# Kernel tuning notes

Measured on AMD Instinct MI355X. Metric: run time of the kernel, lower is better.

## Reference

```python
import jax, jax.numpy as jnp
import numpy as np

T = 0.07        # temperature (hardcoded in CCM)
BN_EPS = 1e-5   # torch BatchNorm1d default eps (eval mode, running stats)


def _l2norm(x):
    # torch F.normalize(dim=1): x / max(||x||, 1e-12)
    n = jnp.linalg.norm(x, axis=1, keepdims=True)
    return x / jnp.maximum(n, 1e-12)


def _attn(q, k):
    # cosine similarity scaled by 1/t and 1/sqrt(num_keys)
    scale = jnp.asarray(k.shape[0], q.dtype) ** 0.5
    return (_l2norm(q) @ _l2norm(k).T) / T / scale


def setup_inputs() -> dict:
    key = jax.random.key(0)
    ks = jax.random.split(key, 24)
    D, N, BS, C, H = 2048, 1024, 64, 65, 128
    f32 = jnp.float32
    def g(k, shape, scale=1.0):
        return jax.random.normal(k, shape, f32) * scale
    return {
        "all_f": g(ks[0], (BS, D)),
        "embedding": _l2norm(g(ks[1], (N, D))),  # memory queue (normalized at init)
        "all_y": jax.random.randint(ks[2], (BS,), 0, C),
        "head_w1": g(ks[3], (D, H), 1.0 / np.sqrt(D)),
        "head_b1": jnp.zeros((H,), f32),
        "head_g": jax.random.uniform(ks[4], (H,), f32) + 0.5,
        "head_beta": g(ks[5], (H,), 0.1),
        "head_rm": g(ks[6], (H,), 0.1),
        "head_rv": jax.random.uniform(ks[7], (H,), f32) + 0.5,
        "head_w2": g(ks[8], (H, H), 1.0 / np.sqrt(H)),
        "head_b2": jnp.zeros((H,), f32),
        "mix_w1": g(ks[9], (2 * H, H), 1.0 / np.sqrt(2 * H)),
        "mix_b1": jnp.zeros((H,), f32),
        "mix_g": jax.random.uniform(ks[10], (H,), f32) + 0.5,
        "mix_beta": g(ks[11], (H,), 0.1),
        "mix_rm": g(ks[12], (H,), 0.1),
        "mix_rv": jax.random.uniform(ks[13], (H,), f32) + 0.5,
        "mix_w2": g(ks[14], (H, D), 1.0 / np.sqrt(H)),
        "mix_b2": jnp.zeros((D,), f32),
        "clf_w": g(ks[15], (D, C), 1.0 / np.sqrt(D)),
        "clf_b": jnp.zeros((C,), f32),
    }


def reference(all_f, embedding, all_y,
              head_w1, head_b1, head_g, head_beta, head_rm, head_rv, head_w2, head_b2,
              mix_w1, mix_b1, mix_g, mix_beta, mix_rm, mix_rv, mix_w2, mix_b2,
              clf_w, clf_b):
    # CCM.causal(all_f, embedding, all_y): returns [bs, num_classes]
    H = head_b2.shape[0]
    # z|x attention over the memory queue
    z_x = jax.nn.softmax(_attn(all_f, embedding), axis=-1)          # [bs, N]

    def head(x):
        h = x @ head_w1 + head_b1
        h = (h - head_rm) * jax.lax.rsqrt(head_rv + BN_EPS) * head_g + head_beta
        return jax.nn.relu(h) @ head_w2 + head_b2                   # [., 128]

    hf = head(all_f)        # [bs, 128]
    hz = head(embedding)    # [N, 128]
    # mixer layer 1 on concat([hf, hz]) decomposed into two matmuls + broadcast add
    h1 = hf @ mix_w1[:H] + mix_b1                                   # [bs, 128]
    h1 = h1[:, None, :] + (hz @ mix_w1[H:])[None, :, :]             # [bs, N, 128]
    h1 = (h1 - mix_rm) * jax.lax.rsqrt(mix_rv + BN_EPS) * mix_g + mix_beta
    h1 = jax.nn.relu(h1)
    mixed = h1 @ mix_w2 + mix_b2                                    # [bs, N, D]
    y_zx = jax.nn.softmax(mixed @ clf_w + clf_b, axis=-1)           # [bs, N, C] = p(y|z,x)
    # p(x): self-attention row-sums, softmax over the batch (all_y given -> this branch)
    p_x = jax.nn.softmax(_attn(all_f, all_f).sum(axis=1), axis=0)   # [bs]
    sum_x = jnp.einsum('b,bnc->nc', p_x, y_zx)                      # [N, C]
    return z_x @ sum_x                                              # [bs, C]
```

## Files before the change

### kernel.cpp

```cpp
#include <hip/hip_runtime.h>
#include <hip/hip_bf16.h>
#include <math.h>

#define D   2048
#define NQ  1024
#define BSZ 64
#define NC  65
#define HD  128

#define OFF_SCALEH 0
#define OFF_CH     128
#define OFF_BZC    256
#define OFF_BAC    384
#define OFF_BVEC   512
#define OFF_PXP    640
#define OFF_WC     896
#define OFF_SP     145280
#define OFF_SUMX   669568
#define OFF_FNB    751488
#define OFF_AFB    817024
#define OFF_EMBB   882560
#define OFF_W1T    1931136
#define OFF_WZT    2062208
#define OFF_WAT    2070400
#define OFF_MW2B   2078592
#define OFF_CWT    2226048
#define OFF_H1P    2307968

typedef __attribute__((ext_vector_type(8))) short    bf16x8;
typedef __attribute__((ext_vector_type(4))) float    f32x4;
typedef __attribute__((ext_vector_type(8))) unsigned short u16x8;
typedef __attribute__((ext_vector_type(2))) unsigned short u16x2;

__device__ inline unsigned short f2b(float v) {
    __hip_bfloat16 h = __float2bfloat16(v);
    return __builtin_bit_cast(unsigned short, h);
}
__device__ inline float bf2f(unsigned short u) {
    return __builtin_bit_cast(float, ((unsigned)u) << 16);
}

__global__ void __launch_bounds__(256) k_prep(const float* __restrict__ all_f,
                                              const float* __restrict__ emb,
                                              const float* __restrict__ head_w1,
                                              const float* __restrict__ head_b1,
                                              const float* __restrict__ head_g,
                                              const float* __restrict__ head_beta,
                                              const float* __restrict__ head_rm,
                                              const float* __restrict__ head_rv,
                                              const float* __restrict__ head_w2,
                                              const float* __restrict__ head_b2,
                                              const float* __restrict__ mix_w1,
                                              const float* __restrict__ mix_b1,
                                              const float* __restrict__ mix_g,
                                              const float* __restrict__ mix_beta,
                                              const float* __restrict__ mix_rm,
                                              const float* __restrict__ mix_rv,
                                              const float* __restrict__ mix_w2,
                                              const float* __restrict__ mix_b2,
                                              const float* __restrict__ clf_w,
                                              float* __restrict__ ws) {
    __shared__ float sbuf[128*66];
    int bid = blockIdx.x, t = threadIdx.x;
    if (bid == 0) {
        int h = t & 127, jq = t >> 7;
        float sb = 0.f, sa = 0.f;
        #pragma unroll 8
        for (int j = jq*64; j < jq*64 + 64; ++j) {
            float b2v = head_b2[j];
            sb = fmaf(b2v, mix_w1[(HD + j)*HD + h], sb);
            sa = fmaf(b2v, mix_w1[j*HD + h], sa);
        }
        sbuf[jq*256 + h]       = sb;
        sbuf[jq*256 + 128 + h] = sa;
        __syncthreads();
        if (jq == 0) {
            float s = head_g[h] * rsqrtf(head_rv[h] + 1e-5f);
            ws[OFF_SCALEH + h] = s;
            ws[OFF_CH + h] = (head_b1[h] - head_rm[h]) * s + head_beta[h];
            float ms = mix_g[h] * rsqrtf(mix_rv[h] + 1e-5f);
            float msh = mix_beta[h] - mix_rm[h] * ms;
            float sbT = sbuf[h] + sbuf[256 + h];
            float saT = sbuf[128 + h] + sbuf[256 + 128 + h];
            ws[OFF_BZC + h] = sbT * ms;
            ws[OFF_BAC + h] = fmaf(saT + mix_b1[h], ms, msh);
        }
    } else if (bid < 129) {
        int j = bid - 1;
        int h = t & 127, which = t >> 7;
        const float* M1 = mix_w1 + (which ? 0 : HD*HD);
        float ms = mix_g[h] * rsqrtf(mix_rv[h] + 1e-5f);
        float acc = 0.f;
        #pragma unroll 8
        for (int k = 0; k < HD; ++k)
            acc = fmaf(head_w2[j*HD + k], M1[k*HD + h], acc);
        unsigned short* dst = (unsigned short*)(ws + (which ? OFF_WAT : OFF_WZT));
        dst[h*HD + j] = f2b(acc * ms);
    } else if (bid < 165) {
        int r0 = (bid - 129) * 4;
        unsigned short* dst = (unsigned short*)(ws + OFF_MW2B);
        int i0 = t * 8;
        for (int rr = 0; rr < 4; ++rr) {
            int r = r0 + rr;
            u16x8 o;
            if (r < HD || r == HD) {
                const float* src = (r < HD) ? (mix_w2 + (size_t)r * D) : mix_b2;
                float4 f1 = *(const float4*)(src + i0);
                float4 f2 = *(const float4*)(src + i0 + 4);
                o[0]=f2b(f1.x); o[1]=f2b(f1.y); o[2]=f2b(f1.z); o[3]=f2b(f1.w);
                o[4]=f2b(f2.x); o[5]=f2b(f2.y); o[6]=f2b(f2.z); o[7]=f2b(f2.w);
            } else {
                o[0]=0;o[1]=0;o[2]=0;o[3]=0;o[4]=0;o[5]=0;o[6]=0;o[7]=0;
            }
            *(u16x8*)(dst + (size_t)r*D + i0) = o;
        }
    } else if (bid < 181) {
        int k0 = (bid - 165) * 128;
        float (*tile)[66] = (float(*)[66])sbuf;
        for (int i = t; i < 128*65; i += 256) {
            int r = i / 65;
            tile[r][i - 65*r] = clf_w[(size_t)k0*65 + i];
        }
        __syncthreads();
        unsigned short* cwt = (unsigned short*)(ws + OFF_CWT);
        for (int idx = t; idx < 80*16; idx += 256) {
            int c = idx >> 4, kq = idx & 15;
            u16x8 v;
            #pragma unroll
            for (int j = 0; j < 8; ++j)
                v[j] = (c < NC) ? f2b(tile[kq*8 + j][c]) : (unsigned short)0;
            *(u16x8*)(cwt + (size_t)c*D + k0 + kq*8) = v;
        }
    } else if (bid < 245) {
        int b = bid - 181;
        const float* src = all_f + (size_t)b * D;
        int i0 = t * 8;
        float4 f1 = *(const float4*)(src + i0);
        float4 f2 = *(const float4*)(src + i0 + 4);
        float s = f1.x*f1.x + f1.y*f1.y + f1.z*f1.z + f1.w*f1.w
                + f2.x*f2.x + f2.y*f2.y + f2.z*f2.z + f2.w*f2.w;
        s += __shfl_xor(s, 1);  s += __shfl_xor(s, 2);  s += __shfl_xor(s, 4);
        s += __shfl_xor(s, 8);  s += __shfl_xor(s, 16); s += __shfl_xor(s, 32);
        if ((t & 63) == 0) sbuf[t >> 6] = s;
        __syncthreads();
        float tot = sbuf[0] + sbuf[1] + sbuf[2] + sbuf[3];
        float rn = 1.f / fmaxf(sqrtf(tot), 1e-12f);
        unsigned short* fnb = (unsigned short*)(ws + OFF_FNB) + (size_t)b * D;
        unsigned short* afb = (unsigned short*)(ws + OFF_AFB) + (size_t)b * D;
        u16x8 on, oa;
        on[0]=f2b(f1.x*rn); on[1]=f2b(f1.y*rn); on[2]=f2b(f1.z*rn); on[3]=f2b(f1.w*rn);
        on[4]=f2b(f2.x*rn); on[5]=f2b(f2.y*rn); on[6]=f2b(f2.z*rn); on[7]=f2b(f2.w*rn);
        oa[0]=f2b(f1.x); oa[1]=f2b(f1.y); oa[2]=f2b(f1.z); oa[3]=f2b(f1.w);
        oa[4]=f2b(f2.x); oa[5]=f2b(f2.y); oa[6]=f2b(f2.z); oa[7]=f2b(f2.w);
        *(u16x8*)(fnb + i0) = on;
        *(u16x8*)(afb + i0) = oa;
    } else if (bid < 757) {
        int n0 = (bid - 245) * 2;
        unsigned short* dst = (unsigned short*)(ws + OFF_EMBB);
        int i0 = t * 8;
        for (int r = 0; r < 2; ++r) {
            const float* src = emb + (size_t)(n0 + r) * D;
            float4 f1 = *(const float4*)(src + i0);
            float4 f2 = *(const float4*)(src + i0 + 4);
            u16x8 o;
            o[0]=f2b(f1.x); o[1]=f2b(f1.y); o[2]=f2b(f1.z); o[3]=f2b(f1.w);
            o[4]=f2b(f2.x); o[5]=f2b(f2.y); o[6]=f2b(f2.z); o[7]=f2b(f2.w);
            *(u16x8*)(dst + (size_t)(n0 + r)*D + i0) = o;
        }
    } else {
        int rb = bid - 757;
        float (*tile)[33] = (float(*)[33])sbuf;
        int k0 = (rb >> 2) * 128, h0 = (rb & 3) * 32;
        int hh = t & 31, kk = t >> 5;
        for (int r = 0; r < 16; ++r)
            tile[kk + r*8][hh] = head_w1[(size_t)(k0 + kk + r*8)*HD + h0 + hh];
        __syncthreads();
        unsigned short* dst = (unsigned short*)(ws + OFF_W1T);
        int kcol = (t & 63) * 2, hrow = t >> 6;
        for (int r = 0; r < 8; ++r) {
            int h = hrow + r*4;
            u16x2 v;
            v[0] = f2b(tile[kcol][h]);
            v[1] = f2b(tile[kcol + 1][h]);
            *(u16x2*)(dst + (size_t)(h0 + h)*D + k0 + kcol) = v;
        }
    }
}

__global__ void __launch_bounds__(512) k_main(const float* __restrict__ clf_b,
                                              float* __restrict__ ws) {
    __shared__ float part[2][32][128];
    __shared__ float wcp[8][16][16];
    int bid = blockIdx.x, t = threadIdx.x;
    int lane = t & 63, wv = t >> 6;
    int row16 = lane & 15, kgrp = lane >> 4;
    if (bid < 128) {
        const unsigned short* fnb  = (const unsigned short*)(ws + OFF_FNB);
        const unsigned short* embb = (const unsigned short*)(ws + OFF_EMBB);
        int nt = bid & 15, ks = bid >> 4;
        int b0 = (wv & 3) * 16;
        int n0 = nt*64 + (wv >> 2) * 32;
        const unsigned short* Ap = fnb  + (size_t)(b0 + row16)*D + ks*256 + kgrp*8;
        const unsigned short* B0 = embb + (size_t)(n0 + row16)*D + ks*256 + kgrp*8;
        const unsigned short* B1 = B0 + 16*D;
        f32x4 a0 = {0,0,0,0}, a1 = {0,0,0,0};
        #pragma unroll
        for (int s = 0; s < 8; ++s) {
            bf16x8 a = *(const bf16x8*)(Ap + s*32);
            a0 = __builtin_amdgcn_mfma_f32_16x16x32_bf16(a, *(const bf16x8*)(B0 + s*32), a0, 0, 0, 0);
            a1 = __builtin_amdgcn_mfma_f32_16x16x32_bf16(a, *(const bf16x8*)(B1 + s*32), a1, 0, 0, 0);
        }
        float* Sp = ws + OFF_SP + (size_t)ks * BSZ * NQ;
        #pragma unroll
        for (int r = 0; r < 4; ++r) {
            float* rowp = Sp + (size_t)(b0 + kgrp*4 + r)*NQ + n0;
            rowp[row16]      = a0[r];
            rowp[16 + row16] = a1[r];
        }
    } else if (bid < 196) {
        int role = bid - 128;
        int tile = role >> 1, kh = role & 1;
        bool isF = tile >= 32;
        const unsigned short* Arow = isF
            ? (const unsigned short*)(ws + OFF_AFB) + (size_t)(tile - 32) * 32 * D
            : (const unsigned short*)(ws + OFF_EMBB) + (size_t)tile * 32 * D;
        const unsigned short* w1t = (const unsigned short*)(ws + OFF_W1T);
        int hgrp = wv & 3, kq = wv >> 2;
        int koff = kh*1024 + kq*512;
        const unsigned short* Ap = Arow + (size_t)row16*D + koff + kgrp*8;
        const unsigned short* B0 = w1t + (size_t)(hgrp*32 + row16)*D + koff + kgrp*8;
        const unsigned short* B1 = B0 + 16*D;
        f32x4 h00 = {0,0,0,0}, h01 = {0,0,0,0}, h10 = {0,0,0,0}, h11 = {0,0,0,0};
        #pragma unroll 4
        for (int s = 0; s < 16; ++s) {
            bf16x8 a0 = *(const bf16x8*)(Ap + s*32);
            bf16x8 a1 = *(const bf16x8*)(Ap + 16*D + s*32);
            bf16x8 b0 = *(const bf16x8*)(B0 + s*32);
            bf16x8 b1 = *(const bf16x8*)(B1 + s*32);
            h00 = __builtin_amdgcn_mfma_f32_16x16x32_bf16(a0, b0, h00, 0, 0, 0);
            h01 = __builtin_amdgcn_mfma_f32_16x16x32_bf16(a0, b1, h01, 0, 0, 0);
            h10 = __builtin_amdgcn_mfma_f32_16x16x32_bf16(a1, b0, h10, 0, 0, 0);
            h11 = __builtin_amdgcn_mfma_f32_16x16x32_bf16(a1, b1, h11, 0, 0, 0);
        }
        int mb = kgrp*4, hc0 = hgrp*32 + row16, hc1 = hc0 + 16;
        #pragma unroll
        for (int r = 0; r < 4; ++r) {
            part[kq][mb + r][hc0]      = h00[r];
            part[kq][mb + r][hc1]      = h01[r];
            part[kq][16 + mb + r][hc0] = h10[r];
            part[kq][16 + mb + r][hc1] = h11[r];
        }
        __syncthreads();
        int row = t >> 4, c8 = (t & 15) * 8;
        float* dst = ws + OFF_H1P + (size_t)kh*1088*HD + (size_t)(tile*32 + row)*HD + c8;
        float4 o0, o1;
        o0.x = part[0][row][c8+0] + part[1][row][c8+0];
        o0.y = part[0][row][c8+1] + part[1][row][c8+1];
        o0.z = part[0][row][c8+2] + part[1][row][c8+2];
        o0.w = part[0][row][c8+3] + part[1][row][c8+3];
        o1.x = part[0][row][c8+4] + part[1][row][c8+4];
        o1.y = part[0][row][c8+5] + part[1][row][c8+5];
        o1.z = part[0][row][c8+6] + part[1][row][c8+6];
        o1.w = part[0][row][c8+7] + part[1][row][c8+7];
        *(float4*)dst = o0;
        *(float4*)(dst + 4) = o1;
    } else if (bid < 241) {
        int w = bid - 196;
        int mt = w / 5, ntile = w % 5;
        const unsigned short* mw2b = (const unsigned short*)(ws + OFF_MW2B);
        const unsigned short* cwt  = (const unsigned short*)(ws + OFF_CWT);
        const unsigned short* Ap = mw2b + (size_t)(mt*16 + row16)*D + wv*256 + kgrp*8;
        const unsigned short* Bp = cwt  + (size_t)(ntile*16 + row16)*D + wv*256 + kgrp*8;
        f32x4 acc = {0,0,0,0};
        #pragma unroll
        for (int s = 0; s < 8; ++s)
            acc = __builtin_amdgcn_mfma_f32_16x16x32_bf16(
                *(const bf16x8*)(Ap + s*32), *(const bf16x8*)(Bp + s*32), acc, 0, 0, 0);
        #pragma unroll
        for (int r = 0; r < 4; ++r)
            wcp[wv][kgrp*4 + r][row16] = acc[r];
        __syncthreads();
        if (t < 256) {
            int j = t >> 4, c16 = t & 15;
            float s = 0.f;
            #pragma unroll
            for (int q = 0; q < 8; ++q) s += wcp[q][j][c16];
            int jj = mt*16 + j, c = ntile*16 + c16;
            unsigned short* wct = (unsigned short*)(ws + OFF_WC);
            if (jj < HD)       wct[(size_t)c*HD + jj] = f2b(s);
            else if (jj == HD) ws[OFF_BVEC + c] = (c < NC) ? s + clf_b[c] : -1e30f;
        }
    } else {
        int pb = bid - 241;
        const unsigned short* fnb = (const unsigned short*)(ws + OFF_FNB);
        int bq = wv & 3, kq = (wv >> 2) + pb*2;
        int b0 = bq*16;
        const unsigned short* Ap = fnb + (size_t)(b0 + row16)*D + kq*512 + kgrp*8;
        const unsigned short* Bp = fnb + (size_t)row16*D + kq*512 + kgrp*8;
        f32x4 acc[4];
        #pragma unroll
        for (int nt = 0; nt < 4; ++nt) acc[nt] = (f32x4){0.f,0.f,0.f,0.f};
        #pragma unroll 2
        for (int s = 0; s < 16; ++s) {
            bf16x8 a = *(const bf16x8*)(Ap + s*32);
            #pragma unroll
            for (int nt = 0; nt < 4; ++nt)
                acc[nt] = __builtin_amdgcn_mfma_f32_16x16x32_bf16(
                    a, *(const bf16x8*)(Bp + (size_t)nt*16*D + s*32), acc[nt], 0, 0, 0);
        }
        #pragma unroll
        for (int r = 0; r < 4; ++r) {
            float v = acc[0][r] + acc[1][r] + acc[2][r] + acc[3][r];
            v += __shfl_xor(v, 1); v += __shfl_xor(v, 2);
            v += __shfl_xor(v, 4); v += __shfl_xor(v, 8);
            if (row16 == 0)
                ws[OFF_PXP + kq*64 + b0 + kgrp*4 + r] = v;
        }
    }
}

__global__ void __launch_bounds__(512, 4) k_mixfin(const float* __restrict__ ws,
                                                   float* __restrict__ wsw) {
    __shared__ unsigned short wcs[80][136];
    __shared__ unsigned short ushA[96][136];
    __shared__ unsigned short a2s[64][136];
    __shared__ unsigned short b2s[32][136];
    __shared__ float redp[8][80];
    int bid = blockIdx.x, t = threadIdx.x;
    int lane = t & 63, wv = t >> 6;
    int row16 = lane & 15, kgrp = lane >> 4;

    const unsigned short* wct = (const unsigned short*)(ws + OFF_WC);
    for (int i = t; i < 80*16; i += 512) {
        int r = i >> 4, cc = (i & 15) * 8;
        *(u16x8*)&wcs[r][cc] = *(const u16x8*)(wct + (size_t)r*HD + cc);
    }

    int tb = bid >> 4;
    int frow = t >> 4, fc8 = (t & 15) * 8;
    #pragma unroll
    for (int g = 0; g < 3; ++g) {
        int u = frow + g*32;
        int h1row = (u < 32) ? (tb*32 + u) : (1024 + (u - 32));
        const float* h0p = ws + OFF_H1P + (size_t)h1row*HD + fc8;
        const float* h1p = h0p + (size_t)1088*HD;
        #pragma unroll
        for (int j = 0; j < 8; ++j) {
            int col = fc8 + j;
            float v = h0p[j] + h1p[j];
            ushA[u][col] = f2b(fmaxf(fmaf(v, ws[OFF_SCALEH + col], ws[OFF_CH + col]), 0.f));
        }
    }

    const float invTS = 1.0f / (0.07f * 8.0f);
    float sv = (ws[OFF_PXP + lane] + ws[OFF_PXP + 64 + lane]
              + ws[OFF_PXP + 128 + lane] + ws[OFF_PXP + 192 + lane]) * invTS;
    float m2 = sv;
    m2 = fmaxf(m2, __shfl_xor(m2, 1));  m2 = fmaxf(m2, __shfl_xor(m2, 2));
    m2 = fmaxf(m2, __shfl_xor(m2, 4));  m2 = fmaxf(m2, __shfl_xor(m2, 8));
    m2 = fmaxf(m2, __shfl_xor(m2, 16)); m2 = fmaxf(m2, __shfl_xor(m2, 32));
    float e2 = __expf(sv - m2);
    float ssum = e2;
    ssum += __shfl_xor(ssum, 1);  ssum += __shfl_xor(ssum, 2);  ssum += __shfl_xor(ssum, 4);
    ssum += __shfl_xor(ssum, 8);  ssum += __shfl_xor(ssum, 16); ssum += __shfl_xor(ssum, 32);
    float px = e2 / ssum;
    float bvl[5];
    #pragma unroll
    for (int ct = 0; ct < 5; ++ct) bvl[ct] = ws[OFF_BVEC + ct*16 + row16];
    __syncthreads();

    #pragma unroll
    for (int i = 0; i < 3; ++i) {
        int task = wv + i*8;
        int rt6 = task >> 2, cg = task & 3;
        bool isF = rt6 >= 2;
        const unsigned short* wt = (const unsigned short*)(ws + (isF ? OFF_WAT : OFF_WZT));
        const unsigned short* W0 = wt + (size_t)(cg*32 + row16)*HD + kgrp*8;
        const unsigned short* W1b = W0 + 16*HD;
        f32x4 o0 = {0,0,0,0}, o1 = {0,0,0,0};
        #pragma unroll
        for (int s = 0; s < 4; ++s) {
            bf16x8 a = *(const bf16x8*)(&ushA[rt6*16 + row16][s*32 + kgrp*8]);
            o0 = __builtin_amdgcn_mfma_f32_16x16x32_bf16(a, *(const bf16x8*)(W0 + s*32), o0, 0, 0, 0);
            o1 = __builtin_amdgcn_mfma_f32_16x16x32_bf16(a, *(const bf16x8*)(W1b + s*32), o1, 0, 0, 0);
        }
        int hcA = cg*32 + row16, hcB = hcA + 16;
        int boff = isF ? OFF_BAC : OFF_BZC;
        float bz0 = ws[boff + hcA], bz1 = ws[boff + hcB];
        #pragma unroll
        for (int r = 0; r < 4; ++r) {
            int orow = rt6*16 + kgrp*4 + r;
            if (orow < 32) {
                b2s[orow][hcA] = f2b(o0[r] + bz0);
                b2s[orow][hcB] = f2b(o1[r] + bz1);
            } else {
                a2s[orow - 32][hcA] = f2b(o0[r] + bz0);
                a2s[orow - 32][hcB] = f2b(o1[r] + bz1);
            }
        }
    }
    __syncthreads();

    int bt = wv & 3, ng = wv >> 2;
    u16x8 a2f[4];
    #pragma unroll
    for (int kt = 0; kt < 4; ++kt)
        a2f[kt] = *(const u16x8*)&a2s[bt*16 + row16][kt*32 + kgrp*8];
    int b2row = (bid & 15)*2 + ng;
    bf16x8 af[4];
    #pragma unroll
    for (int kt = 0; kt < 4; ++kt) {
        u16x8 bv = *(const u16x8*)&b2s[b2row][kt*32 + kgrp*8];
        bf16x8 v;
        #pragma unroll
        for (int j = 0; j < 8; ++j)
            v[j] = (short)f2b(fmaxf(bf2f(a2f[kt][j]) + bf2f(bv[j]), 0.f));
        af[kt] = v;
    }
    f32x4 acc[5];
    #pragma unroll
    for (int ct = 0; ct < 5; ++ct) acc[ct] = (f32x4){0.f,0.f,0.f,0.f};
    #pragma unroll
    for (int ct = 0; ct < 5; ++ct)
        #pragma unroll
        for (int kt = 0; kt < 4; ++kt)
            acc[ct] = __builtin_amdgcn_mfma_f32_16x16x32_bf16(
                af[kt], *(const bf16x8*)(&wcs[ct*16 + row16][kt*32 + kgrp*8]),
                acc[ct], 0, 0, 0);
    float outp[5] = {0.f, 0.f, 0.f, 0.f, 0.f};
    #pragma unroll
    for (int r = 0; r < 4; ++r) {
        float v0 = acc[0][r] + bvl[0];
        float v1 = acc[1][r] + bvl[1];
        float v2 = acc[2][r] + bvl[2];
        float v3 = acc[3][r] + bvl[3];
        float v4 = acc[4][r] + bvl[4];
        float m = fmaxf(fmaxf(fmaxf(v0, v1), fmaxf(v2, v3)), v4);
        m = fmaxf(m, __shfl_xor(m, 1)); m = fmaxf(m, __shfl_xor(m, 2));
        m = fmaxf(m, __shfl_xor(m, 4)); m = fmaxf(m, __shfl_xor(m, 8));
        float e0 = __expf(v0 - m), e1 = __expf(v1 - m), e2v = __expf(v2 - m);
        float e3 = __expf(v3 - m), e4 = __expf(v4 - m);
        float s = e0 + e1 + e2v + e3 + e4;
        s += __shfl_xor(s, 1); s += __shfl_xor(s, 2);
        s += __shfl_xor(s, 4); s += __shfl_xor(s, 8);
        float pxr = __shfl(px, bt*16 + kgrp*4 + r);
        float scale = pxr / s;
        outp[0] = fmaf(e0, scale, outp[0]);
        outp[1] = fmaf(e1, scale, outp[1]);
        outp[2] = fmaf(e2v, scale, outp[2]);
        outp[3] = fmaf(e3, scale, outp[3]);
        outp[4] = fmaf(e4, scale, outp[4]);
    }
    #pragma unroll
    for (int ct = 0; ct < 5; ++ct) {
        float v = outp[ct];
        v += __shfl_xor(v, 16); v += __shfl_xor(v, 32);
        outp[ct] = v;
    }
    if (kgrp == 0) {
        #pragma unroll
        for (int ct = 0; ct < 5; ++ct) redp[wv][ct*16 + row16] = outp[ct];
    }
    __syncthreads();
    if (t < 160) {
        int half = (t >= 80) ? 1 : 0;
        int c = t - 80*half;
        int nn = bid*2 + half;
        wsw[OFF_SUMX + (size_t)nn*80 + c] =
            redp[half*4 + 0][c] + redp[half*4 + 1][c]
          + redp[half*4 + 2][c] + redp[half*4 + 3][c];
    }
}

__global__ void __launch_bounds__(512) k_outz(const float* __restrict__ ws, float* __restrict__ out) {
    __shared__ float red8s[8];
    __shared__ float zrow[NQ];
    __shared__ float parts[8][20];
    int bid = blockIdx.x, t = threadIdx.x;
    int lane = t & 63, wvv = t >> 6;
    int b = bid >> 2, cq = bid & 3;
    const float invTS = 1.0f / (0.07f * 32.0f);
    const float* Sp = ws + OFF_SP + (size_t)b * NQ;
    float s0 = 0.f, s1 = 0.f;
    #pragma unroll
    for (int p = 0; p < 8; ++p) {
        s0 += Sp[(size_t)p*BSZ*NQ + t];
        s1 += Sp[(size_t)p*BSZ*NQ + 512 + t];
    }
    float e0 = __expf(s0 * invTS), e1 = __expf(s1 * invTS);
    float ss = e0 + e1;
    ss += __shfl_xor(ss, 1);  ss += __shfl_xor(ss, 2);  ss += __shfl_xor(ss, 4);
    ss += __shfl_xor(ss, 8);  ss += __shfl_xor(ss, 16); ss += __shfl_xor(ss, 32);
    if (lane == 0) red8s[wvv] = ss;
    __syncthreads();
    float S = red8s[0] + red8s[1] + red8s[2] + red8s[3]
            + red8s[4] + red8s[5] + red8s[6] + red8s[7];
    float inv = 1.f / S;
    zrow[t]       = e0 * inv;
    zrow[512 + t] = e1 * inv;
    __syncthreads();
    const float* Sx = ws + OFF_SUMX;
    int nbase = wvv * 128;
    if (lane < 20) {
        int c = cq*20 + lane;
        float a0 = 0.f;
        #pragma unroll 8
        for (int k = 0; k < 128; ++k)
            a0 = fmaf(zrow[nbase + k], Sx[(size_t)(nbase + k)*80 + c], a0);
        parts[wvv][lane] = a0;
    }
    __syncthreads();
    if (t < 20) {
        int cg = cq*20 + t;
        if (cg < NC) {
            float s = 0.f;
            #pragma unroll
            for (int q = 0; q < 8; ++q) s += parts[q][t];
            out[b*NC + cg] = s;
        }
    }
}

extern "C" void kernel_launch(void* const* d_in, const int* in_sizes, int n_in,
                              void* d_out, int out_size, void* d_ws, size_t ws_size,
                              hipStream_t stream) {
    const float* all_f    = (const float*)d_in[0];
    const float* emb      = (const float*)d_in[1];
    const float* head_w1  = (const float*)d_in[3];
    const float* head_b1  = (const float*)d_in[4];
    const float* head_g   = (const float*)d_in[5];
    const float* head_beta= (const float*)d_in[6];
    const float* head_rm  = (const float*)d_in[7];
    const float* head_rv  = (const float*)d_in[8];
    const float* head_w2  = (const float*)d_in[9];
    const float* head_b2  = (const float*)d_in[10];
    const float* mix_w1   = (const float*)d_in[11];
    const float* mix_b1   = (const float*)d_in[12];
    const float* mix_g    = (const float*)d_in[13];
    const float* mix_beta = (const float*)d_in[14];
    const float* mix_rm   = (const float*)d_in[15];
    const float* mix_rv   = (const float*)d_in[16];
    const float* mix_w2   = (const float*)d_in[17];
    const float* mix_b2   = (const float*)d_in[18];
    const float* clf_w    = (const float*)d_in[19];
    const float* clf_b    = (const float*)d_in[20];
    float* ws  = (float*)d_ws;
    float* out = (float*)d_out;

    hipLaunchKernelGGL(k_prep, dim3(821), dim3(256), 0, stream,
                       all_f, emb, head_w1, head_b1, head_g, head_beta, head_rm, head_rv,
                       head_w2, head_b2, mix_w1, mix_b1, mix_g, mix_beta, mix_rm, mix_rv,
                       mix_w2, mix_b2, clf_w, ws);
    hipLaunchKernelGGL(k_main,   dim3(243), dim3(512), 0, stream, clf_b, ws);
    hipLaunchKernelGGL(k_mixfin, dim3(512), dim3(512), 0, stream, ws, ws);
    hipLaunchKernelGGL(k_outz,   dim3(256), dim3(512), 0, stream, ws, out);
}
```

Baseline: 59.37 us.

## Fuse final z_x reduction into mixer kernel via atomic ticket and spin-wait

Merges the separate output kernel into the mixer kernel. Each block takes an atomic ticket when it finishes, and the last 64 blocks to finish spin until all 512 have written sum_x, then each computes one batch row of the output. The counter is reset in k_main. This removes one kernel launch and its inter-kernel gap. It also reworks the final dot product so one block covers all 65 classes instead of four blocks of 20. The risks are spin-waiting blocks holding CUs, and the ticket scheme depends on forward progress of the other blocks.

```diff
diff --git a/kernel.cpp b/kernel.cpp
--- a/kernel.cpp
+++ b/kernel.cpp
@@ -13,6 +13,7 @@
 #define OFF_BZC    256
 #define OFF_BAC    384
 #define OFF_BVEC   512
+#define OFF_TICK   600
 #define OFF_PXP    640
 #define OFF_WC     896
 #define OFF_SP     145280
@@ -292,6 +293,7 @@
         }
     } else {
         int pb = bid - 241;
+        if (pb == 0 && t == 0) *(unsigned*)(ws + OFF_TICK) = 0u;
         const unsigned short* fnb = (const unsigned short*)(ws + OFF_FNB);
         int bq = wv & 3, kq = (wv >> 2) + pb*2;
         int b0 = bq*16;
@@ -319,13 +321,24 @@
     }
 }
 
-__global__ void __launch_bounds__(512, 4) k_mixfin(const float* __restrict__ ws,
-                                                   float* __restrict__ wsw) {
-    __shared__ unsigned short wcs[80][136];
-    __shared__ unsigned short ushA[96][136];
-    __shared__ unsigned short a2s[64][136];
-    __shared__ unsigned short b2s[32][136];
-    __shared__ float redp[8][80];
+__global__ void __launch_bounds__(512, 4) k_mixz(float* __restrict__ ws,
+                                                 float* __restrict__ out) {
+    union SU {
+        struct {
+            unsigned short wcs[80][136];
+            unsigned short ushA[96][136];
+            unsigned short a2s[64][136];
+            unsigned short b2s[32][136];
+            float redp[8][80];
+        } m;
+        struct {
+            float red8s[8];
+            float zrow[NQ];
+            float parts[8][128];
+        } f;
+    };
+    __shared__ SU su;
+    __shared__ unsigned tk_s;
     int bid = blockIdx.x, t = threadIdx.x;
     int lane = t & 63, wv = t >> 6;
     int row16 = lane & 15, kgrp = lane >> 4;
@@ -333,7 +346,7 @@
     const unsigned short* wct = (const unsigned short*)(ws + OFF_WC);
     for (int i = t; i < 80*16; i += 512) {
         int r = i >> 4, cc = (i & 15) * 8;
-        *(u16x8*)&wcs[r][cc] = *(const u16x8*)(wct + (size_t)r*HD + cc);
+        *(u16x8*)&su.m.wcs[r][cc] = *(const u16x8*)(wct + (size_t)r*HD + cc);
     }
 
     int tb = bid >> 4;
@@ -348,7 +361,7 @@
         for (int j = 0; j < 8; ++j) {
             int col = fc8 + j;
             float v = h0p[j] + h1p[j];
-            ushA[u][col] = f2b(fmaxf(fmaf(v, ws[OFF_SCALEH + col], ws[OFF_CH + col]), 0.f));
+            su.m.ushA[u][col] = f2b(fmaxf(fmaf(v, ws[OFF_SCALEH + col], ws[OFF_CH + col]), 0.f));
         }
     }
 
@@ -380,7 +393,7 @@
         f32x4 o0 = {0,0,0,0}, o1 = {0,0,0,0};
         #pragma unroll
         for (int s = 0; s < 4; ++s) {
-            bf16x8 a = *(const bf16x8*)(&ushA[rt6*16 + row16][s*32 + kgrp*8]);
+            bf16x8 a = *(const bf16x8*)(&su.m.ushA[rt6*16 + row16][s*32 + kgrp*8]);
             o0 = __builtin_amdgcn_mfma_f32_16x16x32_bf16(a, *(const bf16x8*)(W0 + s*32), o0, 0, 0, 0);
             o1 = __builtin_amdgcn_mfma_f32_16x16x32_bf16(a, *(const bf16x8*)(W1b + s*32), o1, 0, 0, 0);
         }
@@ -391,11 +404,11 @@
         for (int r = 0; r < 4; ++r) {
             int orow = rt6*16 + kgrp*4 + r;
             if (orow < 32) {
-                b2s[orow][hcA] = f2b(o0[r] + bz0);
-                b2s[orow][hcB] = f2b(o1[r] + bz1);
+                su.m.b2s[orow][hcA] = f2b(o0[r] + bz0);
+                su.m.b2s[orow][hcB] = f2b(o1[r] + bz1);
             } else {
-                a2s[orow - 32][hcA] = f2b(o0[r] + bz0);
-                a2s[orow - 32][hcB] = f2b(o1[r] + bz1);
+                su.m.a2s[orow - 32][hcA] = f2b(o0[r] + bz0);
+                su.m.a2s[orow - 32][hcB] = f2b(o1[r] + bz1);
             }
         }
     }
@@ -405,12 +418,12 @@
     u16x8 a2f[4];
     #pragma unroll
     for (int kt = 0; kt < 4; ++kt)
-        a2f[kt] = *(const u16x8*)&a2s[bt*16 + row16][kt*32 + kgrp*8];
+        a2f[kt] = *(const u16x8*)&su.m.a2s[bt*16 + row16][kt*32 + kgrp*8];
     int b2row = (bid & 15)*2 + ng;
     bf16x8 af[4];
     #pragma unroll
     for (int kt = 0; kt < 4; ++kt) {
-        u16x8 bv = *(const u16x8*)&b2s[b2row][kt*32 + kgrp*8];
+        u16x8 bv = *(const u16x8*)&su.m.b2s[b2row][kt*32 + kgrp*8];
         bf16x8 v;
         #pragma unroll
         for (int j = 0; j < 8; ++j)
@@ -425,7 +438,7 @@
         #pragma unroll
         for (int kt = 0; kt < 4; ++kt)
             acc[ct] = __builtin_amdgcn_mfma_f32_16x16x32_bf16(
-                af[kt], *(const bf16x8*)(&wcs[ct*16 + row16][kt*32 + kgrp*8]),
+                af[kt], *(const bf16x8*)(&su.m.wcs[ct*16 + row16][kt*32 + kgrp*8]),
                 acc[ct], 0, 0, 0);
     float outp[5] = {0.f, 0.f, 0.f, 0.f, 0.f};
     #pragma unroll
@@ -459,27 +472,34 @@
     }
     if (kgrp == 0) {
         #pragma unroll
-        for (int ct = 0; ct < 5; ++ct) redp[wv][ct*16 + row16] = outp[ct];
+        for (int ct = 0; ct < 5; ++ct) su.m.redp[wv][ct*16 + row16] = outp[ct];
     }
     __syncthreads();
     if (t < 160) {
         int half = (t >= 80) ? 1 : 0;
         int c = t - 80*half;
         int nn = bid*2 + half;
-        wsw[OFF_SUMX + (size_t)nn*80 + c] =
-            redp[half*4 + 0][c] + redp[half*4 + 1][c]
-          + redp[half*4 + 2][c] + redp[half*4 + 3][c];
-    }
-}
-
-__global__ void __launch_bounds__(512) k_outz(const float* __restrict__ ws, float* __restrict__ out) {
-    __shared__ float red8s[8];
-    __shared__ float zrow[NQ];
-    __shared__ float parts[8][20];
-    int bid = blockIdx.x, t = threadIdx.x;
-    int lane = t & 63, wvv = t >> 6;
-    int b = bid >> 2, cq = bid & 3;
-    const float invTS = 1.0f / (0.07f * 32.0f);
+        ws[OFF_SUMX + (size_t)nn*80 + c] =
+            su.m.redp[half*4 + 0][c] + su.m.redp[half*4 + 1][c]
+          + su.m.redp[half*4 + 2][c] + su.m.redp[half*4 + 3][c];
+    }
+
+    __syncthreads();
+    if (t == 0)
+        tk_s = __hip_atomic_fetch_add((unsigned*)(ws + OFF_TICK), 1u,
+                                      __ATOMIC_ACQ_REL, __HIP_MEMORY_SCOPE_AGENT);
+    __syncthreads();
+    unsigned old = tk_s;
+    if (old < 448u) return;
+    if (t == 0) {
+        while (__hip_atomic_load((unsigned*)(ws + OFF_TICK),
+                                 __ATOMIC_ACQUIRE, __HIP_MEMORY_SCOPE_AGENT) < 512u)
+            __builtin_amdgcn_s_sleep(2);
+    }
+    __syncthreads();
+
+    int b = (int)old - 448;
+    const float invTS2 = 1.0f / (0.07f * 32.0f);
     const float* Sp = ws + OFF_SP + (size_t)b * NQ;
     float s0 = 0.f, s1 = 0.f;
     #pragma unroll
@@ -487,37 +507,37 @@
         s0 += Sp[(size_t)p*BSZ*NQ + t];
         s1 += Sp[(size_t)p*BSZ*NQ + 512 + t];
     }
-    float e0 = __expf(s0 * invTS), e1 = __expf(s1 * invTS);
+    float e0 = __expf(s0 * invTS2), e1 = __expf(s1 * invTS2);
     float ss = e0 + e1;
     ss += __shfl_xor(ss, 1);  ss += __shfl_xor(ss, 2);  ss += __shfl_xor(ss, 4);
     ss += __shfl_xor(ss, 8);  ss += __shfl_xor(ss, 16); ss += __shfl_xor(ss, 32);
-    if (lane == 0) red8s[wvv] = ss;
-    __syncthreads();
-    float S = red8s[0] + red8s[1] + red8s[2] + red8s[3]
-            + red8s[4] + red8s[5] + red8s[6] + red8s[7];
+    if (lane == 0) su.f.red8s[wv] = ss;
+    __syncthreads();
+    float S = su.f.red8s[0] + su.f.red8s[1] + su.f.red8s[2] + su.f.red8s[3]
+            + su.f.red8s[4] + su.f.red8s[5] + su.f.red8s[6] + su.f.red8s[7];
     float inv = 1.f / S;
-    zrow[t]       = e0 * inv;
-    zrow[512 + t] = e1 * inv;
+    su.f.zrow[t]       = e0 * inv;
+    su.f.zrow[512 + t] = e1 * inv;
     __syncthreads();
     const float* Sx = ws + OFF_SUMX;
-    int nbase = wvv * 128;
-    if (lane < 20) {
-        int c = cq*20 + lane;
-        float a0 = 0.f;
-        #pragma unroll 8
-        for (int k = 0; k < 128; ++k)
-            a0 = fmaf(zrow[nbase + k], Sx[(size_t)(nbase + k)*80 + c], a0);
-        parts[wvv][lane] = a0;
-    }
-    __syncthreads();
-    if (t < 20) {
-        int cg = cq*20 + t;
-        if (cg < NC) {
-            float s = 0.f;
-            #pragma unroll
-            for (int q = 0; q < 8; ++q) s += parts[q][t];
-            out[b*NC + cg] = s;
-        }
+    int c2 = 64 + (lane & 15);
+    int nbase = wv * 128;
+    float a0 = 0.f, a1 = 0.f;
+    #pragma unroll 8
+    for (int k = 0; k < 128; ++k) {
+        float z = su.f.zrow[nbase + k];
+        const float* srow = Sx + (size_t)(nbase + k) * 80;
+        a0 = fmaf(z, srow[lane], a0);
+        a1 = fmaf(z, srow[c2], a1);
+    }
+    su.f.parts[wv][lane] = a0;
+    if (lane < 16) su.f.parts[wv][64 + lane] = a1;
+    __syncthreads();
+    if (t < NC) {
+        float s = 0.f;
+        #pragma unroll
+        for (int q = 0; q < 8; ++q) s += su.f.parts[q][t];
+        out[b*NC + t] = s;
     }
 }
 
@@ -551,7 +571,6 @@
                        all_f, emb, head_w1, head_b1, head_g, head_beta, head_rm, head_rv,
                        head_w2, head_b2, mix_w1, mix_b1, mix_g, mix_beta, mix_rm, mix_rv,
                        mix_w2, mix_b2, clf_w, ws);
-    hipLaunchKernelGGL(k_main,   dim3(243), dim3(512), 0, stream, clf_b, ws);
-    hipLaunchKernelGGL(k_mixfin, dim3(512), dim3(512), 0, stream, ws, ws);
-    hipLaunchKernelGGL(k_outz,   dim3(256), dim3(512), 0, stream, ws, out);
+    hipLaunchKernelGGL(k_main, dim3(243), dim3(512), 0, stream, clf_b, ws);
+    hipLaunchKernelGGL(k_mixz, dim3(512), dim3(512), 0, stream, ws, out);
 }
```

Result: slower. 69.31 us (+16.7%).

## Move head second layer into k_main and simplify mixer kernel

Applied to the files above, without the earlier changes.

The head's first-layer blocks in k_main now cover the full K range per tile (34 blocks instead of 68 split-K blocks). They apply BN+ReLU and the 128x128 second projection in place, writing fp32 A2/B2 rows to the workspace. The mixer kernel no longer recomputes the BN/ReLU and the second-layer matmul in each of its 512 blocks. It now runs as 256 blocks that each handle 4 queue entries in two passes, which removes heavy redundant per-block work and large shared-memory staging. The cost is less parallelism in the first-layer GEMM (fewer blocks, longer K loops) and an extra serial matmul stage inside k_main.

```diff
diff --git a/kernel.cpp b/kernel.cpp
--- a/kernel.cpp
+++ b/kernel.cpp
@@ -15,6 +15,8 @@
 #define OFF_BVEC   512
 #define OFF_PXP    640
 #define OFF_WC     896
+#define OFF_A2T    6016
+#define OFF_B2     14208
 #define OFF_SP     145280
 #define OFF_SUMX   669568
 #define OFF_FNB    751488
@@ -25,7 +27,6 @@
 #define OFF_WAT    2070400
 #define OFF_MW2B   2078592
 #define OFF_CWT    2226048
-#define OFF_H1P    2307968
 
 typedef __attribute__((ext_vector_type(8))) short    bf16x8;
 typedef __attribute__((ext_vector_type(4))) float    f32x4;
@@ -35,9 +36,6 @@
 __device__ inline unsigned short f2b(float v) {
     __hip_bfloat16 h = __float2bfloat16(v);
     return __builtin_bit_cast(unsigned short, h);
-}
-__device__ inline float bf2f(unsigned short u) {
-    return __builtin_bit_cast(float, ((unsigned)u) << 16);
 }
 
 __global__ void __launch_bounds__(256) k_prep(const float* __restrict__ all_f,
@@ -190,6 +188,7 @@
 __global__ void __launch_bounds__(512) k_main(const float* __restrict__ clf_b,
                                               float* __restrict__ ws) {
     __shared__ float part[2][32][128];
+    __shared__ unsigned short ush[32][136];
     __shared__ float wcp[8][16][16];
     int bid = blockIdx.x, t = threadIdx.x;
     int lane = t & 63, wv = t >> 6;
@@ -217,22 +216,20 @@
             rowp[row16]      = a0[r];
             rowp[16 + row16] = a1[r];
         }
-    } else if (bid < 196) {
-        int role = bid - 128;
-        int tile = role >> 1, kh = role & 1;
+    } else if (bid < 162) {
+        int tile = bid - 128;
         bool isF = tile >= 32;
         const unsigned short* Arow = isF
             ? (const unsigned short*)(ws + OFF_AFB) + (size_t)(tile - 32) * 32 * D
             : (const unsigned short*)(ws + OFF_EMBB) + (size_t)tile * 32 * D;
         const unsigned short* w1t = (const unsigned short*)(ws + OFF_W1T);
-        int hgrp = wv & 3, kq = wv >> 2;
-        int koff = kh*1024 + kq*512;
-        const unsigned short* Ap = Arow + (size_t)row16*D + koff + kgrp*8;
-        const unsigned short* B0 = w1t + (size_t)(hgrp*32 + row16)*D + koff + kgrp*8;
+        int hgrp = wv & 3, kh = wv >> 2;
+        const unsigned short* Ap = Arow + (size_t)row16*D + kh*1024 + kgrp*8;
+        const unsigned short* B0 = w1t + (size_t)(hgrp*32 + row16)*D + kh*1024 + kgrp*8;
         const unsigned short* B1 = B0 + 16*D;
         f32x4 h00 = {0,0,0,0}, h01 = {0,0,0,0}, h10 = {0,0,0,0}, h11 = {0,0,0,0};
         #pragma unroll 4
-        for (int s = 0; s < 16; ++s) {
+        for (int s = 0; s < 32; ++s) {
             bf16x8 a0 = *(const bf16x8*)(Ap + s*32);
             bf16x8 a1 = *(const bf16x8*)(Ap + 16*D + s*32);
             bf16x8 b0 = *(const bf16x8*)(B0 + s*32);
@@ -245,27 +242,48 @@
         int mb = kgrp*4, hc0 = hgrp*32 + row16, hc1 = hc0 + 16;
         #pragma unroll
         for (int r = 0; r < 4; ++r) {
-            part[kq][mb + r][hc0]      = h00[r];
-            part[kq][mb + r][hc1]      = h01[r];
-            part[kq][16 + mb + r][hc0] = h10[r];
-            part[kq][16 + mb + r][hc1] = h11[r];
-        }
-        __syncthreads();
-        int row = t >> 4, c8 = (t & 15) * 8;
-        float* dst = ws + OFF_H1P + (size_t)kh*1088*HD + (size_t)(tile*32 + row)*HD + c8;
-        float4 o0, o1;
-        o0.x = part[0][row][c8+0] + part[1][row][c8+0];
-        o0.y = part[0][row][c8+1] + part[1][row][c8+1];
-        o0.z = part[0][row][c8+2] + part[1][row][c8+2];
-        o0.w = part[0][row][c8+3] + part[1][row][c8+3];
-        o1.x = part[0][row][c8+4] + part[1][row][c8+4];
-        o1.y = part[0][row][c8+5] + part[1][row][c8+5];
-        o1.z = part[0][row][c8+6] + part[1][row][c8+6];
-        o1.w = part[0][row][c8+7] + part[1][row][c8+7];
-        *(float4*)dst = o0;
-        *(float4*)(dst + 4) = o1;
-    } else if (bid < 241) {
-        int w = bid - 196;
+            part[kh][mb + r][hc0]      = h00[r];
+            part[kh][mb + r][hc1]      = h01[r];
+            part[kh][16 + mb + r][hc0] = h10[r];
+            part[kh][16 + mb + r][hc1] = h11[r];
+        }
+        __syncthreads();
+        {
+            int row = t >> 4, cg = (t & 15) * 8;
+            #pragma unroll
+            for (int j = 0; j < 8; ++j) {
+                int col = cg + j;
+                float v = part[0][row][col] + part[1][row][col];
+                ush[row][col] = f2b(fmaxf(fmaf(v, ws[OFF_SCALEH + col], ws[OFF_CH + col]), 0.f));
+            }
+        }
+        __syncthreads();
+        {
+            int rt = wv >> 2, wv2 = wv & 3;
+            const unsigned short* wt = (const unsigned short*)(ws + (isF ? OFF_WAT : OFF_WZT));
+            const unsigned short* W0 = wt + (size_t)(wv2*32 + row16)*HD + kgrp*8;
+            const unsigned short* W1b = W0 + 16*HD;
+            f32x4 o0 = {0,0,0,0}, o1 = {0,0,0,0};
+            #pragma unroll
+            for (int s = 0; s < 4; ++s) {
+                bf16x8 a = *(const bf16x8*)(&ush[rt*16 + row16][s*32 + kgrp*8]);
+                o0 = __builtin_amdgcn_mfma_f32_16x16x32_bf16(a, *(const bf16x8*)(W0 + s*32), o0, 0, 0, 0);
+                o1 = __builtin_amdgcn_mfma_f32_16x16x32_bf16(a, *(const bf16x8*)(W1b + s*32), o1, 0, 0, 0);
+            }
+            int hcA = wv2*32 + row16, hcB = hcA + 16;
+            int boff = isF ? OFF_BAC : OFF_BZC;
+            float bz0 = ws[boff + hcA], bz1 = ws[boff + hcB];
+            float* outp = isF ? (ws + OFF_A2T + (size_t)(tile - 32)*32*HD)
+                              : (ws + OFF_B2  + (size_t)tile*32*HD);
+            int mb2 = kgrp*4;
+            #pragma unroll
+            for (int r = 0; r < 4; ++r) {
+                outp[(size_t)(rt*16 + mb2 + r)*HD + hcA] = o0[r] + bz0;
+                outp[(size_t)(rt*16 + mb2 + r)*HD + hcB] = o1[r] + bz1;
+            }
+        }
+    } else if (bid < 207) {
+        int w = bid - 162;
         int mt = w / 5, ntile = w % 5;
         const unsigned short* mw2b = (const unsigned short*)(ws + OFF_MW2B);
         const unsigned short* cwt  = (const unsigned short*)(ws + OFF_CWT);
@@ -291,7 +309,7 @@
             else if (jj == HD) ws[OFF_BVEC + c] = (c < NC) ? s + clf_b[c] : -1e30f;
         }
     } else {
-        int pb = bid - 241;
+        int pb = bid - 207;
         const unsigned short* fnb = (const unsigned short*)(ws + OFF_FNB);
         int bq = wv & 3, kq = (wv >> 2) + pb*2;
         int b0 = bq*16;
@@ -319,39 +337,18 @@
     }
 }
 
-__global__ void __launch_bounds__(512, 4) k_mixfin(const float* __restrict__ ws,
-                                                   float* __restrict__ wsw) {
+__global__ void __launch_bounds__(512) k_mix(const float* __restrict__ ws,
+                                             float* __restrict__ wsw) {
     __shared__ unsigned short wcs[80][136];
-    __shared__ unsigned short ushA[96][136];
-    __shared__ unsigned short a2s[64][136];
-    __shared__ unsigned short b2s[32][136];
     __shared__ float redp[8][80];
     int bid = blockIdx.x, t = threadIdx.x;
     int lane = t & 63, wv = t >> 6;
     int row16 = lane & 15, kgrp = lane >> 4;
-
     const unsigned short* wct = (const unsigned short*)(ws + OFF_WC);
     for (int i = t; i < 80*16; i += 512) {
         int r = i >> 4, cc = (i & 15) * 8;
         *(u16x8*)&wcs[r][cc] = *(const u16x8*)(wct + (size_t)r*HD + cc);
     }
-
-    int tb = bid >> 4;
-    int frow = t >> 4, fc8 = (t & 15) * 8;
-    #pragma unroll
-    for (int g = 0; g < 3; ++g) {
-        int u = frow + g*32;
-        int h1row = (u < 32) ? (tb*32 + u) : (1024 + (u - 32));
-        const float* h0p = ws + OFF_H1P + (size_t)h1row*HD + fc8;
-        const float* h1p = h0p + (size_t)1088*HD;
-        #pragma unroll
-        for (int j = 0; j < 8; ++j) {
-            int col = fc8 + j;
-            float v = h0p[j] + h1p[j];
-            ushA[u][col] = f2b(fmaxf(fmaf(v, ws[OFF_SCALEH + col], ws[OFF_CH + col]), 0.f));
-        }
-    }
-
     const float invTS = 1.0f / (0.07f * 8.0f);
     float sv = (ws[OFF_PXP + lane] + ws[OFF_PXP + 64 + lane]
               + ws[OFF_PXP + 128 + lane] + ws[OFF_PXP + 192 + lane]) * invTS;
@@ -367,108 +364,89 @@
     float bvl[5];
     #pragma unroll
     for (int ct = 0; ct < 5; ++ct) bvl[ct] = ws[OFF_BVEC + ct*16 + row16];
-    __syncthreads();
-
-    #pragma unroll
-    for (int i = 0; i < 3; ++i) {
-        int task = wv + i*8;
-        int rt6 = task >> 2, cg = task & 3;
-        bool isF = rt6 >= 2;
-        const unsigned short* wt = (const unsigned short*)(ws + (isF ? OFF_WAT : OFF_WZT));
-        const unsigned short* W0 = wt + (size_t)(cg*32 + row16)*HD + kgrp*8;
-        const unsigned short* W1b = W0 + 16*HD;
-        f32x4 o0 = {0,0,0,0}, o1 = {0,0,0,0};
-        #pragma unroll
-        for (int s = 0; s < 4; ++s) {
-            bf16x8 a = *(const bf16x8*)(&ushA[rt6*16 + row16][s*32 + kgrp*8]);
-            o0 = __builtin_amdgcn_mfma_f32_16x16x32_bf16(a, *(const bf16x8*)(W0 + s*32), o0, 0, 0, 0);
-            o1 = __builtin_amdgcn_mfma_f32_16x16x32_bf16(a, *(const bf16x8*)(W1b + s*32), o1, 0, 0, 0);
-        }
-        int hcA = cg*32 + row16, hcB = hcA + 16;
-        int boff = isF ? OFF_BAC : OFF_BZC;
-        float bz0 = ws[boff + hcA], bz1 = ws[boff + hcB];
-        #pragma unroll
-        for (int r = 0; r < 4; ++r) {
-            int orow = rt6*16 + kgrp*4 + r;
-            if (orow < 32) {
-                b2s[orow][hcA] = f2b(o0[r] + bz0);
-                b2s[orow][hcB] = f2b(o1[r] + bz1);
-            } else {
-                a2s[orow - 32][hcA] = f2b(o0[r] + bz0);
-                a2s[orow - 32][hcB] = f2b(o1[r] + bz1);
-            }
-        }
-    }
-    __syncthreads();
-
     int bt = wv & 3, ng = wv >> 2;
-    u16x8 a2f[4];
-    #pragma unroll
-    for (int kt = 0; kt < 4; ++kt)
-        a2f[kt] = *(const u16x8*)&a2s[bt*16 + row16][kt*32 + kgrp*8];
-    int b2row = (bid & 15)*2 + ng;
-    bf16x8 af[4];
+    const float* a2r = ws + OFF_A2T + (size_t)(bt*16 + row16) * HD;
+    float4 a2lo[4], a2hi[4];
     #pragma unroll
     for (int kt = 0; kt < 4; ++kt) {
-        u16x8 bv = *(const u16x8*)&b2s[b2row][kt*32 + kgrp*8];
-        bf16x8 v;
-        #pragma unroll
-        for (int j = 0; j < 8; ++j)
-            v[j] = (short)f2b(fmaxf(bf2f(a2f[kt][j]) + bf2f(bv[j]), 0.f));
-        af[kt] = v;
-    }
-    f32x4 acc[5];
+        a2lo[kt] = *(const float4*)(a2r + kt*32 + kgrp*8);
+        a2hi[kt] = *(const float4*)(a2r + kt*32 + kgrp*8 + 4);
+    }
+    __syncthreads();
     #pragma unroll
-    for (int ct = 0; ct < 5; ++ct) acc[ct] = (f32x4){0.f,0.f,0.f,0.f};
-    #pragma unroll
-    for (int ct = 0; ct < 5; ++ct)
-        #pragma unroll
-        for (int kt = 0; kt < 4; ++kt)
-            acc[ct] = __builtin_amdgcn_mfma_f32_16x16x32_bf16(
-                af[kt], *(const bf16x8*)(&wcs[ct*16 + row16][kt*32 + kgrp*8]),
-                acc[ct], 0, 0, 0);
-    float outp[5] = {0.f, 0.f, 0.f, 0.f, 0.f};
-    #pragma unroll
-    for (int r = 0; r < 4; ++r) {
-        float v0 = acc[0][r] + bvl[0];
-        float v1 = acc[1][r] + bvl[1];
-        float v2 = acc[2][r] + bvl[2];
-        float v3 = acc[3][r] + bvl[3];
-        float v4 = acc[4][r] + bvl[4];
-        float m = fmaxf(fmaxf(fmaxf(v0, v1), fmaxf(v2, v3)), v4);
-        m = fmaxf(m, __shfl_xor(m, 1)); m = fmaxf(m, __shfl_xor(m, 2));
-        m = fmaxf(m, __shfl_xor(m, 4)); m = fmaxf(m, __shfl_xor(m, 8));
-        float e0 = __expf(v0 - m), e1 = __expf(v1 - m), e2v = __expf(v2 - m);
-        float e3 = __expf(v3 - m), e4 = __expf(v4 - m);
-        float s = e0 + e1 + e2v + e3 + e4;
-        s += __shfl_xor(s, 1); s += __shfl_xor(s, 2);
-        s += __shfl_xor(s, 4); s += __shfl_xor(s, 8);
-        float pxr = __shfl(px, bt*16 + kgrp*4 + r);
-        float scale = pxr / s;
-        outp[0] = fmaf(e0, scale, outp[0]);
-        outp[1] = fmaf(e1, scale, outp[1]);
-        outp[2] = fmaf(e2v, scale, outp[2]);
-        outp[3] = fmaf(e3, scale, outp[3]);
-        outp[4] = fmaf(e4, scale, outp[4]);
-    }
-    #pragma unroll
-    for (int ct = 0; ct < 5; ++ct) {
-        float v = outp[ct];
-        v += __shfl_xor(v, 16); v += __shfl_xor(v, 32);
-        outp[ct] = v;
-    }
-    if (kgrp == 0) {
-        #pragma unroll
-        for (int ct = 0; ct < 5; ++ct) redp[wv][ct*16 + row16] = outp[ct];
-    }
-    __syncthreads();
-    if (t < 160) {
-        int half = (t >= 80) ? 1 : 0;
-        int c = t - 80*half;
-        int nn = bid*2 + half;
-        wsw[OFF_SUMX + (size_t)nn*80 + c] =
-            redp[half*4 + 0][c] + redp[half*4 + 1][c]
-          + redp[half*4 + 2][c] + redp[half*4 + 3][c];
+    for (int pass = 0; pass < 2; ++pass) {
+        int n = bid*4 + pass*2 + ng;
+        const float* b2r = ws + OFF_B2 + (size_t)n * HD;
+        bf16x8 af[4];
+        #pragma unroll
+        for (int kt = 0; kt < 4; ++kt) {
+            float4 blo = *(const float4*)(b2r + kt*32 + kgrp*8);
+            float4 bhi = *(const float4*)(b2r + kt*32 + kgrp*8 + 4);
+            bf16x8 v;
+            v[0] = (short)f2b(fmaxf(a2lo[kt].x + blo.x, 0.f));
+            v[1] = (short)f2b(fmaxf(a2lo[kt].y + blo.y, 0.f));
+            v[2] = (short)f2b(fmaxf(a2lo[kt].z + blo.z, 0.f));
+            v[3] = (short)f2b(fmaxf(a2lo[kt].w + blo.w, 0.f));
+            v[4] = (short)f2b(fmaxf(a2hi[kt].x + bhi.x, 0.f));
+            v[5] = (short)f2b(fmaxf(a2hi[kt].y + bhi.y, 0.f));
+            v[6] = (short)f2b(fmaxf(a2hi[kt].z + bhi.z, 0.f));
+            v[7] = (short)f2b(fmaxf(a2hi[kt].w + bhi.w, 0.f));
+            af[kt] = v;
+        }
+        f32x4 acc[5];
+        #pragma unroll
+        for (int ct = 0; ct < 5; ++ct) acc[ct] = (f32x4){0.f,0.f,0.f,0.f};
+        #pragma unroll
+        for (int ct = 0; ct < 5; ++ct)
+            #pragma unroll
+            for (int kt = 0; kt < 4; ++kt)
+                acc[ct] = __builtin_amdgcn_mfma_f32_16x16x32_bf16(
+                    af[kt], *(const bf16x8*)(&wcs[ct*16 + row16][kt*32 + kgrp*8]),
+                    acc[ct], 0, 0, 0);
+        float outp[5] = {0.f, 0.f, 0.f, 0.f, 0.f};
+        #pragma unroll
+        for (int r = 0; r < 4; ++r) {
+            float v0 = acc[0][r] + bvl[0];
+            float v1 = acc[1][r] + bvl[1];
+            float v2 = acc[2][r] + bvl[2];
+            float v3 = acc[3][r] + bvl[3];
+            float v4 = acc[4][r] + bvl[4];
+            float m = fmaxf(fmaxf(fmaxf(v0, v1), fmaxf(v2, v3)), v4);
+            m = fmaxf(m, __shfl_xor(m, 1)); m = fmaxf(m, __shfl_xor(m, 2));
+            m = fmaxf(m, __shfl_xor(m, 4)); m = fmaxf(m, __shfl_xor(m, 8));
+            float e0 = __expf(v0 - m), e1 = __expf(v1 - m), e2v = __expf(v2 - m);
+            float e3 = __expf(v3 - m), e4 = __expf(v4 - m);
+            float s = e0 + e1 + e2v + e3 + e4;
+            s += __shfl_xor(s, 1); s += __shfl_xor(s, 2);
+            s += __shfl_xor(s, 4); s += __shfl_xor(s, 8);
+            float pxr = __shfl(px, bt*16 + kgrp*4 + r);
+            float scale = pxr / s;
+            outp[0] = fmaf(e0, scale, outp[0]);
+            outp[1] = fmaf(e1, scale, outp[1]);
+            outp[2] = fmaf(e2v, scale, outp[2]);
+            outp[3] = fmaf(e3, scale, outp[3]);
+            outp[4] = fmaf(e4, scale, outp[4]);
+        }
+        #pragma unroll
+        for (int ct = 0; ct < 5; ++ct) {
+            float v = outp[ct];
+            v += __shfl_xor(v, 16); v += __shfl_xor(v, 32);
+            outp[ct] = v;
+        }
+        if (kgrp == 0) {
+            #pragma unroll
+            for (int ct = 0; ct < 5; ++ct) redp[wv][ct*16 + row16] = outp[ct];
+        }
+        __syncthreads();
+        if (t < 160) {
+            int half = (t >= 80) ? 1 : 0;
+            int c = t - 80*half;
+            int nn = bid*4 + pass*2 + half;
+            wsw[OFF_SUMX + (size_t)nn*80 + c] =
+                redp[half*4 + 0][c] + redp[half*4 + 1][c]
+              + redp[half*4 + 2][c] + redp[half*4 + 3][c];
+        }
+        __syncthreads();
     }
 }
 
@@ -551,7 +529,7 @@
                        all_f, emb, head_w1, head_b1, head_g, head_beta, head_rm, head_rv,
                        head_w2, head_b2, mix_w1, mix_b1, mix_g, mix_beta, mix_rm, mix_rv,
                        mix_w2, mix_b2, clf_w, ws);
-    hipLaunchKernelGGL(k_main,   dim3(243), dim3(512), 0, stream, clf_b, ws);
-    hipLaunchKernelGGL(k_mixfin, dim3(512), dim3(512), 0, stream, ws, ws);
-    hipLaunchKernelGGL(k_outz,   dim3(256), dim3(512), 0, stream, ws, out);
+    hipLaunchKernelGGL(k_main, dim3(209), dim3(512), 0, stream, clf_b, ws);
+    hipLaunchKernelGGL(k_mix,  dim3(256), dim3(512), 0, stream, ws, ws);
+    hipLaunchKernelGGL(k_outz, dim3(256), dim3(512), 0, stream, ws, out);
 }
```

After: 65.30 us. 10.0% more time.
